# Kernel optimization log

Measured on AMD Instinct MI355X. Metric: run time of the kernel, lower is better.

Reference implementation:

```python
import jax, jax.numpy as jnp
import numpy as np

SPARSITY = 0.8
NEG_INF = -1e10


def setup_inputs() -> dict:
    key = jax.random.key(0)
    k1, k2 = jax.random.split(key)
    B, N, C = 8, 2048, 768
    x = jax.random.normal(k1, (B, N, C), dtype=jnp.float32)
    # torch nn.Linear weight layout: [out_features, in_features] = [3C, C]
    Wqkv = jax.random.normal(k2, (3 * C, C), dtype=jnp.float32) * (1.0 / np.sqrt(C))
    return {"x": x, "Wqkv": Wqkv}


def reference(x, Wqkv):
    B, N, C = x.shape
    qkv = jnp.einsum('bnc,dc->bnd', x, Wqkv)  # [B, N, 3C]
    Q, K, V = jnp.split(qkv, 3, axis=-1)
    attn = jnp.einsum('bnc,bmc->bnm', Q, K) / jnp.sqrt(jnp.float32(C))  # [B,N,N]
    k = int(N * SPARSITY)
    _, idx = jax.lax.top_k(attn, k)  # [B, N, k]
    b_ix = jnp.arange(B)[:, None, None]
    n_ix = jnp.arange(N)[None, :, None]
    mask = jnp.zeros((B, N, N), dtype=bool).at[b_ix, n_ix, idx].set(True)
    attn = jnp.where(mask, attn, jnp.float32(NEG_INF))
    attn = jax.nn.softmax(attn, axis=-1)
    return jnp.einsum('bnm,bmc->bnc', attn, V)
```

## Files before the change

kernel.cpp:

```cpp
#include <hip/hip_runtime.h>
#include <hip/hip_bf16.h>
#include <math.h>


#define BM 256
#define BN 256
#define BK 64
#define NTHREADS 512

typedef __attribute__((ext_vector_type(8))) short bf16x8;
typedef __attribute__((ext_vector_type(4))) float f32x4;

__device__ __forceinline__ unsigned short f2bf(float f) {
    unsigned u = __float_as_uint(f);
    unsigned r = u + 0x7FFFu + ((u >> 16) & 1u);
    return (unsigned short)(r >> 16);
}
__device__ __forceinline__ float bf2f(unsigned short h) {
    return __uint_as_float(((unsigned)h) << 16);
}

__device__ __forceinline__ void async16(const void* g, void* l) {
    __builtin_amdgcn_global_load_lds(
        (const __attribute__((address_space(1))) void*)g,
        (__attribute__((address_space(3))) void*)l, 16, 0, 0);
}

struct GemmArgs {
    const unsigned short* A0;
    const unsigned short* B0;
    const unsigned short* A0b;
    int zsplit;
    int lda, ldb;
    long batchA, batchB;
    int K;
    float alpha;
};

template <int EPI>
__global__ __launch_bounds__(NTHREADS) void gemm_bf16(
    GemmArgs g, void* Cp0, int ldc, long batchC)
{
    __shared__ unsigned short As[2][BM * BK];
    __shared__ unsigned short Bs[2][BM * BK];

    const int t    = threadIdx.x;
    const int wid  = t >> 6, lane = t & 63;
    const int wr   = wid >> 2, wc = wid & 3;
    const int fr   = lane & 15, fq = lane >> 4;
    const int m0   = blockIdx.y * BM, n0 = blockIdx.x * BN;
    const int z    = blockIdx.z;

    const unsigned short* gA0 = g.A0;
    long zA = (long)z * g.batchA;
    if (g.zsplit && z >= g.zsplit) { gA0 = g.A0b; zA = (long)(z - g.zsplit) * g.batchA; }
    const long zB = (long)z * g.batchB;

    const int srow  = wid * 8 + (lane >> 3);
    const int sgcol = ((lane & 7) ^ (lane >> 3)) * 8;

    f32x4 acc[8][4];
#pragma unroll
    for (int m = 0; m < 8; ++m)
#pragma unroll
        for (int n = 0; n < 4; ++n) acc[m][n] = (f32x4)0.f;

    const int nt = g.K / BK;

    int  sg  = 0;
    long sk0 = 0;
    const unsigned short* sA = gA0 + zA + (long)m0 * g.lda;
    const unsigned short* sB = g.B0 + zB + (long)n0 * g.ldb;

    auto STAGE_GROUP = [&]() {
        if (sg < 4 * nt) {
            const int u  = (sg >> 2) & 1;
            const int gp = sg & 3;
            if (gp < 2) {
                char* lb = (char*)&Bs[u][0] + wid * 1024 + gp * 16384;
                const unsigned short* pb = sB + sk0 + sgcol;
                async16(pb + (long)(srow + gp * 128     ) * g.ldb, lb);
                async16(pb + (long)(srow + gp * 128 + 64) * g.ldb, lb + 8192);
            } else {
                const int ap = gp - 2;
                char* la = (char*)&As[u][0] + wid * 1024 + ap * 16384;
                const unsigned short* pa = sA + sk0 + sgcol;
                async16(pa + (long)(srow + ap * 128     ) * g.lda, la);
                async16(pa + (long)(srow + ap * 128 + 64) * g.lda, la + 8192);
            }
            ++sg;
            if ((sg & 3) == 0) sk0 += BK;
        }
    };

    STAGE_GROUP(); STAGE_GROUP(); STAGE_GROUP();
    STAGE_GROUP(); STAGE_GROUP(); STAGE_GROUP();
    asm volatile("s_waitcnt vmcnt(4)" ::: "memory");
    __builtin_amdgcn_sched_barrier(0);
    __builtin_amdgcn_s_barrier();
    __builtin_amdgcn_sched_barrier(0);

    bf16x8 fA[4][2], fB[4][2];

    for (int tt = 0; tt < nt; ++tt) {
        const unsigned short* Ab = &As[tt & 1][0];
        const unsigned short* Bb = &Bs[tt & 1][0];

        auto LDA4 = [&](int mbase) {
#pragma unroll
            for (int mi = 0; mi < 4; ++mi) {
                const int rr = wr * 128 + (mbase + mi) * 16 + fr;
                fA[mi][0] = *(const bf16x8*)&Ab[rr * 64 + ((fq    ) ^ (rr & 7)) * 8];
                fA[mi][1] = *(const bf16x8*)&Ab[rr * 64 + ((fq + 4) ^ (rr & 7)) * 8];
            }
        };
        auto LDB2 = [&](int nbase) {
#pragma unroll
            for (int ni = 0; ni < 2; ++ni) {
                const int rr = wc * 64 + (nbase + ni) * 16 + fr;
                fB[nbase + ni][0] = *(const bf16x8*)&Bb[rr * 64 + ((fq    ) ^ (rr & 7)) * 8];
                fB[nbase + ni][1] = *(const bf16x8*)&Bb[rr * 64 + ((fq + 4) ^ (rr & 7)) * 8];
            }
        };
        auto MFMA16 = [&](int mq, int nq) {
            __builtin_amdgcn_s_setprio(1);
#pragma unroll
            for (int mi = 0; mi < 4; ++mi)
#pragma unroll
                for (int ni = 0; ni < 2; ++ni)
#pragma unroll
                    for (int ks = 0; ks < 2; ++ks)
                        acc[mq * 4 + mi][nq * 2 + ni] =
                            __builtin_amdgcn_mfma_f32_16x16x32_bf16(
                                fA[mi][ks], fB[nq * 2 + ni][ks],
                                acc[mq * 4 + mi][nq * 2 + ni], 0, 0, 0);
            __builtin_amdgcn_s_setprio(0);
        };
        auto BAR = [&]() {
            __builtin_amdgcn_sched_barrier(0);
            __builtin_amdgcn_s_barrier();
            __builtin_amdgcn_sched_barrier(0);
        };
        auto LGKM0 = [&]() {
            asm volatile("s_waitcnt lgkmcnt(0)" ::: "memory");
            __builtin_amdgcn_sched_barrier(0);
        };

        LDA4(0); LDB2(0);
        STAGE_GROUP();
        BAR(); LGKM0();
        MFMA16(0, 0);
        BAR();

        LDB2(2);
        STAGE_GROUP();
        BAR(); LGKM0();
        MFMA16(0, 1);
        BAR();

        LDA4(4);
        STAGE_GROUP();
        BAR(); LGKM0();
        MFMA16(1, 0);
        BAR();

        STAGE_GROUP();
        BAR();
        MFMA16(1, 1);
        if (tt >= nt - 2) {
            asm volatile("s_waitcnt vmcnt(0)" ::: "memory");
        } else {
            asm volatile("s_waitcnt vmcnt(4)" ::: "memory");
        }
        BAR();
    }

#pragma unroll
    for (int m = 0; m < 8; ++m) {
        const int gr0 = m0 + wr * 128 + m * 16 + fq * 4;
#pragma unroll
        for (int n = 0; n < 4; ++n) {
            const int gc = n0 + wc * 64 + n * 16 + fr;
            if (EPI == 0) {
                float* Cf = (float*)Cp0 + (long)z * batchC;
#pragma unroll
                for (int j = 0; j < 4; ++j)
                    Cf[(long)(gr0 + j) * ldc + gc] = g.alpha * acc[m][n][j];
            } else if (EPI == 3) {
                unsigned short* H = (unsigned short*)Cp0;
#pragma unroll
                for (int j = 0; j < 4; ++j)
                    H[(long)(gr0 + j) * ldc + gc] = f2bf(acc[m][n][j]);
            } else if (EPI == 4) {
                unsigned short* H = (unsigned short*)Cp0 + (long)z * batchC;
#pragma unroll
                for (int j = 0; j < 4; ++j)
                    H[(long)(gr0 + j) * ldc + gc] = f2bf(g.alpha * acc[m][n][j]);
            } else {
                unsigned short* Vt = (unsigned short*)Cp0;
                ushort4 p;
                p.x = f2bf(acc[m][n][0]); p.y = f2bf(acc[m][n][1]);
                p.z = f2bf(acc[m][n][2]); p.w = f2bf(acc[m][n][3]);
                const long idx = ((long)(gr0 >> 11) * 768 + gc) * 2048 + (gr0 & 2047);
                *(ushort4*)&Vt[idx] = p;
            }
        }
    }
}

__global__ __launch_bounds__(256) void cast_bf16(
    const float* __restrict__ in, unsigned short* __restrict__ outp, int n8)
{
    const int i = blockIdx.x * 256 + threadIdx.x;
    if (i >= n8) return;
    const float4 a = ((const float4*)in)[i * 2];
    const float4 b = ((const float4*)in)[i * 2 + 1];
    ushort4 h0, h1;
    h0.x = f2bf(a.x); h0.y = f2bf(a.y); h0.z = f2bf(a.z); h0.w = f2bf(a.w);
    h1.x = f2bf(b.x); h1.y = f2bf(b.y); h1.z = f2bf(b.z); h1.w = f2bf(b.w);
    ((ushort4*)outp)[i * 2]     = h0;
    ((ushort4*)outp)[i * 2 + 1] = h1;
}

#define ROWN 2048

__global__ __launch_bounds__(256) void topk_softmax_rows(
    const unsigned short* __restrict__ Sb, unsigned short* __restrict__ P,
    int kkeep)
{
    __shared__ __align__(16) unsigned hist[2048];
    __shared__ float    redmax[4], redmin[4], ssum[4];
    __shared__ unsigned wsum[4];
    __shared__ unsigned selBin;

    const unsigned short* row = Sb + (long)blockIdx.x * ROWN;
    unsigned short* prow = P + (long)blockIdx.x * ROWN;
    const int t    = threadIdx.x;
    const int lane = t & 63, w = t >> 6;

    float x[8];
    {
        const ushort4 a = ((const ushort4*)row)[t * 2];
        const ushort4 b = ((const ushort4*)row)[t * 2 + 1];
        x[0] = bf2f(a.x); x[1] = bf2f(a.y); x[2] = bf2f(a.z); x[3] = bf2f(a.w);
        x[4] = bf2f(b.x); x[5] = bf2f(b.y); x[6] = bf2f(b.z); x[7] = bf2f(b.w);
    }
    ((uint4*)hist)[t * 2]     = make_uint4(0, 0, 0, 0);
    ((uint4*)hist)[t * 2 + 1] = make_uint4(0, 0, 0, 0);

    float mx = x[0], mn = x[0];
#pragma unroll
    for (int j = 1; j < 8; ++j) { mx = fmaxf(mx, x[j]); mn = fminf(mn, x[j]); }
#pragma unroll
    for (int off = 32; off >= 1; off >>= 1) {
        mx = fmaxf(mx, __shfl_xor(mx, off, 64));
        mn = fminf(mn, __shfl_xor(mn, off, 64));
    }
    if (lane == 0) { redmax[w] = mx; redmin[w] = mn; }
    __syncthreads();
    mx = fmaxf(fmaxf(redmax[0], redmax[1]), fmaxf(redmax[2], redmax[3]));
    mn = fminf(fminf(redmin[0], redmin[1]), fminf(redmin[2], redmin[3]));

    const float scale = 2047.0f / fmaxf(mx - mn, 1e-30f);
    int q[8];
#pragma unroll
    for (int j = 0; j < 8; ++j) {
        int v = (int)((x[j] - mn) * scale);
        q[j] = v < 0 ? 0 : (v > 2047 ? 2047 : v);
        atomicAdd(&hist[q[j]], 1u);
    }
    __syncthreads();

    const uint4 h0 = ((const uint4*)hist)[t * 2];
    const uint4 h1 = ((const uint4*)hist)[t * 2 + 1];
    const unsigned hv[8] = { h0.x, h0.y, h0.z, h0.w, h1.x, h1.y, h1.z, h1.w };
    unsigned loc = 0;
#pragma unroll
    for (int j = 0; j < 8; ++j) loc += hv[j];
    unsigned s = loc;
#pragma unroll
    for (int off = 1; off <= 32; off <<= 1) {
        const unsigned o = __shfl_down(s, off, 64);
        s += (lane + off < 64) ? o : 0u;
    }
    if (lane == 0) wsum[w] = s;
    const unsigned texcl = s - loc;
    __syncthreads();
    unsigned above = texcl;
#pragma unroll
    for (int w2 = 0; w2 < 4; ++w2)
        if (w2 > w) above += wsum[w2];
    {
        unsigned cum = above;
        int hit = -1;
#pragma unroll
        for (int j = 7; j >= 0; --j) {
            const unsigned sp = cum;
            cum += hv[j];
            if (cum >= (unsigned)kkeep && sp < (unsigned)kkeep) hit = 8 * t + j;
        }
        if (hit >= 0) selBin = (unsigned)hit;
    }
    __syncthreads();
    const int bstar = (int)selBin;

    float e[8];
    float sum = 0.f;
#pragma unroll
    for (int j = 0; j < 8; ++j) {
        e[j] = (q[j] >= bstar) ? __expf(x[j] - mx) : 0.f;
        sum += e[j];
    }
#pragma unroll
    for (int off = 32; off >= 1; off >>= 1)
        sum += __shfl_xor(sum, off, 64);
    if (lane == 0) ssum[w] = sum;
    __syncthreads();
    const float inv = 1.0f / (ssum[0] + ssum[1] + ssum[2] + ssum[3]);

    ushort4 o0, o1;
    o0.x = f2bf(e[0] * inv); o0.y = f2bf(e[1] * inv);
    o0.z = f2bf(e[2] * inv); o0.w = f2bf(e[3] * inv);
    o1.x = f2bf(e[4] * inv); o1.y = f2bf(e[5] * inv);
    o1.z = f2bf(e[6] * inv); o1.w = f2bf(e[7] * inv);
    ((ushort4*)prow)[t * 2]     = o0;
    ((ushort4*)prow)[t * 2 + 1] = o1;
}

extern "C" void kernel_launch(void* const* d_in, const int* in_sizes, int n_in,
                              void* d_out, int out_size, void* d_ws, size_t ws_size,
                              hipStream_t stream)
{
    const float* x = (const float*)d_in[0];
    const float* W = (const float*)d_in[1];
    float* out = (float*)d_out;

    const int B = 8, N = 2048, C = 768;
    const int M = B * N;
    const int kkeep = 1638;

    char* ws = (char*)d_ws;
    unsigned short* QKb = (unsigned short*)(ws);
    unsigned short* Vt  = (unsigned short*)(ws + 50331648);
    unsigned short* Sb  = (unsigned short*)(ws + 75497472);
    unsigned short* Pb1 = (unsigned short*)(ws + 109051904);
    unsigned short* Pb2 = (unsigned short*)(ws + 142606336);
    unsigned short* xb  = (unsigned short*)(ws + 75497472);
    unsigned short* Wb  = (unsigned short*)(ws + 75497472 + 25165824);

    cast_bf16<<<dim3(M * C / 8 / 256), 256, 0, stream>>>(x, xb, M * C / 8);
    cast_bf16<<<dim3(3 * C * C / 8 / 256), 256, 0, stream>>>(W, Wb, 3 * C * C / 8);

    {
        GemmArgs pa{};
        pa.lda = C; pa.ldb = C; pa.batchA = 0; pa.batchB = 0;
        pa.K = C; pa.alpha = 1.f; pa.zsplit = 0;
        pa.A0 = xb; pa.B0 = Wb;
        gemm_bf16<3><<<dim3(1536 / BN, M / BM, 1), NTHREADS, 0, stream>>>(
            pa, QKb, 1536, 0);
    }
    {
        GemmArgs pv{};
        pv.lda = C; pv.ldb = C; pv.batchA = 0; pv.batchB = 0;
        pv.K = C; pv.alpha = 1.f; pv.zsplit = 0;
        pv.A0 = xb; pv.B0 = Wb + (size_t)1536 * C;
        gemm_bf16<2><<<dim3(C / BN, M / BM, 1), NTHREADS, 0, stream>>>(
            pv, Vt, 0, 0);
    }
    for (int h = 0; h < 2; ++h) {
        const size_t ho = (size_t)h * 4 * N * 1536;
        GemmArgs qk{};
        qk.lda = 1536; qk.ldb = 1536;
        qk.batchA = (long)N * 1536; qk.batchB = (long)N * 1536; qk.K = C;
        qk.alpha = 1.0f / sqrtf((float)C); qk.zsplit = 0;
        qk.A0 = QKb + ho;
        qk.B0 = QKb + ho + C;
        gemm_bf16<4><<<dim3(N / BN, N / BM, 4), NTHREADS, 0, stream>>>(
            qk, Sb, N, (long)N * N);

        topk_softmax_rows<<<dim3(4 * N), 256, 0, stream>>>(
            Sb, h == 0 ? Pb1 : Pb2, kkeep);
    }
    {
        GemmArgs pvv{};
        pvv.lda = N; pvv.ldb = N;
        pvv.batchA = (long)N * N; pvv.batchB = (long)C * N; pvv.K = N;
        pvv.alpha = 1.f;
        pvv.A0 = Pb1; pvv.A0b = Pb2; pvv.zsplit = 4;
        pvv.B0 = Vt;
        gemm_bf16<0><<<dim3(C / BN, N / BM, 8), NTHREADS, 0, stream>>>(
            pvv, out, C, (long)N * C);
    }
}
```

Baseline: 289.2 us.

## Shrink GEMM tiles to 128x128, fuse QKV projection, add XCD block swizzle

Replaces the 256x256, 8-wave GEMM with a simpler 128x128, 4-wave double-buffered kernel and remaps workgroup IDs round-robin across eight groups, likely to spread tiles across XCDs. The Q/K and V projections are merged into one launch, with an epilogue that writes Q/K row-major and V transposed. The two half-batch QK/top-k passes become a single 8-batch launch of each. This cuts launch count and raises block counts for occupancy, but loses the finer-grained interleaved staging and the larger per-block reuse of the old kernel.

```diff
diff --git a/kernel.cpp b/kernel.cpp
--- a/kernel.cpp
+++ b/kernel.cpp
@@ -3,10 +3,9 @@
 #include <math.h>
 
 
-#define BM 256
-#define BN 256
+#define BM 128
+#define BN 128
 #define BK 64
-#define NTHREADS 512
 
 typedef __attribute__((ext_vector_type(8))) short bf16x8;
 typedef __attribute__((ext_vector_type(4))) float f32x4;
@@ -29,8 +28,6 @@
 struct GemmArgs {
     const unsigned short* A0;
     const unsigned short* B0;
-    const unsigned short* A0b;
-    int zsplit;
     int lda, ldb;
     long batchA, batchB;
     int K;
@@ -38,171 +35,129 @@
 };
 
 template <int EPI>
-__global__ __launch_bounds__(NTHREADS) void gemm_bf16(
-    GemmArgs g, void* Cp0, int ldc, long batchC)
+__global__ __launch_bounds__(256) void gemm_bf16(
+    GemmArgs g, void* Cp0, void* Cp1, int ldc, long batchC)
 {
     __shared__ unsigned short As[2][BM * BK];
-    __shared__ unsigned short Bs[2][BM * BK];
+    __shared__ unsigned short Bs[2][BN * BK];
+
+    const int nx  = gridDim.x, ny = gridDim.y;
+    const int nwg = nx * ny * gridDim.z;
+    const int flat = blockIdx.x + nx * (blockIdx.y + ny * blockIdx.z);
+    const int lid  = (flat & 7) * (nwg >> 3) + (flat >> 3);
+    const int bx   = lid % nx;
+    const int byz  = lid / nx;
+    const int by   = byz % ny;
+    const int bz   = byz / ny;
 
     const int t    = threadIdx.x;
     const int wid  = t >> 6, lane = t & 63;
-    const int wr   = wid >> 2, wc = wid & 3;
+    const int wr   = wid >> 1, wc = wid & 1;
     const int fr   = lane & 15, fq = lane >> 4;
-    const int m0   = blockIdx.y * BM, n0 = blockIdx.x * BN;
-    const int z    = blockIdx.z;
-
-    const unsigned short* gA0 = g.A0;
-    long zA = (long)z * g.batchA;
-    if (g.zsplit && z >= g.zsplit) { gA0 = g.A0b; zA = (long)(z - g.zsplit) * g.batchA; }
-    const long zB = (long)z * g.batchB;
-
-    const int srow  = wid * 8 + (lane >> 3);
-    const int sgcol = ((lane & 7) ^ (lane >> 3)) * 8;
-
-    f32x4 acc[8][4];
-#pragma unroll
-    for (int m = 0; m < 8; ++m)
+    const int m0   = by * BM, n0 = bx * BN;
+
+    const unsigned short* Ab0 = g.A0 + (long)bz * g.batchA + (long)m0 * g.lda;
+    const unsigned short* Bb0 = g.B0 + (long)bz * g.batchB + (long)n0 * g.ldb;
+
+    const int srow = t >> 3;
+    const int sgc  = ((t & 7) ^ (srow & 7)) * 8;
+
+    f32x4 acc[4][4];
+#pragma unroll
+    for (int m = 0; m < 4; ++m)
 #pragma unroll
         for (int n = 0; n < 4; ++n) acc[m][n] = (f32x4)0.f;
 
     const int nt = g.K / BK;
 
-    int  sg  = 0;
-    long sk0 = 0;
-    const unsigned short* sA = gA0 + zA + (long)m0 * g.lda;
-    const unsigned short* sB = g.B0 + zB + (long)n0 * g.ldb;
-
-    auto STAGE_GROUP = [&]() {
-        if (sg < 4 * nt) {
-            const int u  = (sg >> 2) & 1;
-            const int gp = sg & 3;
-            if (gp < 2) {
-                char* lb = (char*)&Bs[u][0] + wid * 1024 + gp * 16384;
-                const unsigned short* pb = sB + sk0 + sgcol;
-                async16(pb + (long)(srow + gp * 128     ) * g.ldb, lb);
-                async16(pb + (long)(srow + gp * 128 + 64) * g.ldb, lb + 8192);
-            } else {
-                const int ap = gp - 2;
-                char* la = (char*)&As[u][0] + wid * 1024 + ap * 16384;
-                const unsigned short* pa = sA + sk0 + sgcol;
-                async16(pa + (long)(srow + ap * 128     ) * g.lda, la);
-                async16(pa + (long)(srow + ap * 128 + 64) * g.lda, la + 8192);
-            }
-            ++sg;
-            if ((sg & 3) == 0) sk0 += BK;
+    auto STAGE = [&](int kt, int u) {
+        const long ko = (long)kt * BK + sgc;
+#pragma unroll
+        for (int i = 0; i < 4; ++i) {
+            async16(Ab0 + (long)(i * 32 + srow) * g.lda + ko,
+                    (char*)&As[u][0] + i * 4096 + wid * 1024);
+            async16(Bb0 + (long)(i * 32 + srow) * g.ldb + ko,
+                    (char*)&Bs[u][0] + i * 4096 + wid * 1024);
         }
     };
 
-    STAGE_GROUP(); STAGE_GROUP(); STAGE_GROUP();
-    STAGE_GROUP(); STAGE_GROUP(); STAGE_GROUP();
-    asm volatile("s_waitcnt vmcnt(4)" ::: "memory");
-    __builtin_amdgcn_sched_barrier(0);
-    __builtin_amdgcn_s_barrier();
-    __builtin_amdgcn_sched_barrier(0);
-
-    bf16x8 fA[4][2], fB[4][2];
+    STAGE(0, 0);
 
     for (int tt = 0; tt < nt; ++tt) {
-        const unsigned short* Ab = &As[tt & 1][0];
-        const unsigned short* Bb = &Bs[tt & 1][0];
-
-        auto LDA4 = [&](int mbase) {
-#pragma unroll
-            for (int mi = 0; mi < 4; ++mi) {
-                const int rr = wr * 128 + (mbase + mi) * 16 + fr;
-                fA[mi][0] = *(const bf16x8*)&Ab[rr * 64 + ((fq    ) ^ (rr & 7)) * 8];
-                fA[mi][1] = *(const bf16x8*)&Ab[rr * 64 + ((fq + 4) ^ (rr & 7)) * 8];
-            }
-        };
-        auto LDB2 = [&](int nbase) {
-#pragma unroll
-            for (int ni = 0; ni < 2; ++ni) {
-                const int rr = wc * 64 + (nbase + ni) * 16 + fr;
-                fB[nbase + ni][0] = *(const bf16x8*)&Bb[rr * 64 + ((fq    ) ^ (rr & 7)) * 8];
-                fB[nbase + ni][1] = *(const bf16x8*)&Bb[rr * 64 + ((fq + 4) ^ (rr & 7)) * 8];
-            }
-        };
-        auto MFMA16 = [&](int mq, int nq) {
-            __builtin_amdgcn_s_setprio(1);
-#pragma unroll
-            for (int mi = 0; mi < 4; ++mi)
-#pragma unroll
-                for (int ni = 0; ni < 2; ++ni)
-#pragma unroll
-                    for (int ks = 0; ks < 2; ++ks)
-                        acc[mq * 4 + mi][nq * 2 + ni] =
-                            __builtin_amdgcn_mfma_f32_16x16x32_bf16(
-                                fA[mi][ks], fB[nq * 2 + ni][ks],
-                                acc[mq * 4 + mi][nq * 2 + ni], 0, 0, 0);
-            __builtin_amdgcn_s_setprio(0);
-        };
-        auto BAR = [&]() {
-            __builtin_amdgcn_sched_barrier(0);
-            __builtin_amdgcn_s_barrier();
-            __builtin_amdgcn_sched_barrier(0);
-        };
-        auto LGKM0 = [&]() {
-            asm volatile("s_waitcnt lgkmcnt(0)" ::: "memory");
-            __builtin_amdgcn_sched_barrier(0);
-        };
-
-        LDA4(0); LDB2(0);
-        STAGE_GROUP();
-        BAR(); LGKM0();
-        MFMA16(0, 0);
-        BAR();
-
-        LDB2(2);
-        STAGE_GROUP();
-        BAR(); LGKM0();
-        MFMA16(0, 1);
-        BAR();
-
-        LDA4(4);
-        STAGE_GROUP();
-        BAR(); LGKM0();
-        MFMA16(1, 0);
-        BAR();
-
-        STAGE_GROUP();
-        BAR();
-        MFMA16(1, 1);
-        if (tt >= nt - 2) {
+        const int cur = tt & 1;
+        if (tt + 1 < nt) {
+            STAGE(tt + 1, cur ^ 1);
+            asm volatile("s_waitcnt vmcnt(8)" ::: "memory");
+        } else {
             asm volatile("s_waitcnt vmcnt(0)" ::: "memory");
-        } else {
-            asm volatile("s_waitcnt vmcnt(4)" ::: "memory");
-        }
-        BAR();
-    }
-
-#pragma unroll
-    for (int m = 0; m < 8; ++m) {
-        const int gr0 = m0 + wr * 128 + m * 16 + fq * 4;
+        }
+        __builtin_amdgcn_sched_barrier(0);
+        __builtin_amdgcn_s_barrier();
+        __builtin_amdgcn_sched_barrier(0);
+
+        const unsigned short* Ab = &As[cur][0];
+        const unsigned short* Bb = &Bs[cur][0];
+        bf16x8 fA[4][2], fB[4][2];
+#pragma unroll
+        for (int m = 0; m < 4; ++m) {
+            const int rr = wr * 64 + m * 16 + fr;
+#pragma unroll
+            for (int ks = 0; ks < 2; ++ks)
+                fA[m][ks] = *(const bf16x8*)&Ab[rr * 64 + ((ks * 4 + fq) ^ (rr & 7)) * 8];
+        }
+#pragma unroll
+        for (int n = 0; n < 4; ++n) {
+            const int rr = wc * 64 + n * 16 + fr;
+#pragma unroll
+            for (int ks = 0; ks < 2; ++ks)
+                fB[n][ks] = *(const bf16x8*)&Bb[rr * 64 + ((ks * 4 + fq) ^ (rr & 7)) * 8];
+        }
+        __builtin_amdgcn_s_setprio(1);
+#pragma unroll
+        for (int m = 0; m < 4; ++m)
+#pragma unroll
+            for (int n = 0; n < 4; ++n)
+#pragma unroll
+                for (int ks = 0; ks < 2; ++ks)
+                    acc[m][n] = __builtin_amdgcn_mfma_f32_16x16x32_bf16(
+                        fA[m][ks], fB[n][ks], acc[m][n], 0, 0, 0);
+        __builtin_amdgcn_s_setprio(0);
+        __builtin_amdgcn_sched_barrier(0);
+        __builtin_amdgcn_s_barrier();
+        __builtin_amdgcn_sched_barrier(0);
+    }
+
+#pragma unroll
+    for (int m = 0; m < 4; ++m) {
+        const int gr0 = m0 + wr * 64 + m * 16 + fq * 4;
 #pragma unroll
         for (int n = 0; n < 4; ++n) {
             const int gc = n0 + wc * 64 + n * 16 + fr;
             if (EPI == 0) {
-                float* Cf = (float*)Cp0 + (long)z * batchC;
+                float* Cf = (float*)Cp0 + (long)bz * batchC;
 #pragma unroll
                 for (int j = 0; j < 4; ++j)
                     Cf[(long)(gr0 + j) * ldc + gc] = g.alpha * acc[m][n][j];
-            } else if (EPI == 3) {
-                unsigned short* H = (unsigned short*)Cp0;
-#pragma unroll
-                for (int j = 0; j < 4; ++j)
-                    H[(long)(gr0 + j) * ldc + gc] = f2bf(acc[m][n][j]);
             } else if (EPI == 4) {
-                unsigned short* H = (unsigned short*)Cp0 + (long)z * batchC;
+                unsigned short* H = (unsigned short*)Cp0 + (long)bz * batchC;
 #pragma unroll
                 for (int j = 0; j < 4; ++j)
                     H[(long)(gr0 + j) * ldc + gc] = f2bf(g.alpha * acc[m][n][j]);
             } else {
-                unsigned short* Vt = (unsigned short*)Cp0;
-                ushort4 p;
-                p.x = f2bf(acc[m][n][0]); p.y = f2bf(acc[m][n][1]);
-                p.z = f2bf(acc[m][n][2]); p.w = f2bf(acc[m][n][3]);
-                const long idx = ((long)(gr0 >> 11) * 768 + gc) * 2048 + (gr0 & 2047);
-                *(ushort4*)&Vt[idx] = p;
+                if (n0 < 1536) {
+                    unsigned short* H = (unsigned short*)Cp0;
+#pragma unroll
+                    for (int j = 0; j < 4; ++j)
+                        H[(long)(gr0 + j) * ldc + gc] = f2bf(acc[m][n][j]);
+                } else {
+                    unsigned short* Vt = (unsigned short*)Cp1;
+                    ushort4 p;
+                    p.x = f2bf(acc[m][n][0]); p.y = f2bf(acc[m][n][1]);
+                    p.z = f2bf(acc[m][n][2]); p.w = f2bf(acc[m][n][3]);
+                    const long idx =
+                        ((long)(gr0 >> 11) * 768 + (gc - 1536)) * 2048 + (gr0 & 2047);
+                    *(ushort4*)&Vt[idx] = p;
+                }
             }
         }
     }
@@ -343,52 +298,39 @@
     unsigned short* QKb = (unsigned short*)(ws);
     unsigned short* Vt  = (unsigned short*)(ws + 50331648);
     unsigned short* Sb  = (unsigned short*)(ws + 75497472);
-    unsigned short* Pb1 = (unsigned short*)(ws + 109051904);
-    unsigned short* Pb2 = (unsigned short*)(ws + 142606336);
+    unsigned short* Pb  = (unsigned short*)(ws + 142606336);
     unsigned short* xb  = (unsigned short*)(ws + 75497472);
-    unsigned short* Wb  = (unsigned short*)(ws + 75497472 + 25165824);
+    unsigned short* Wb  = (unsigned short*)(ws + 100663296);
 
     cast_bf16<<<dim3(M * C / 8 / 256), 256, 0, stream>>>(x, xb, M * C / 8);
     cast_bf16<<<dim3(3 * C * C / 8 / 256), 256, 0, stream>>>(W, Wb, 3 * C * C / 8);
 
     {
         GemmArgs pa{};
+        pa.A0 = xb; pa.B0 = Wb;
         pa.lda = C; pa.ldb = C; pa.batchA = 0; pa.batchB = 0;
-        pa.K = C; pa.alpha = 1.f; pa.zsplit = 0;
-        pa.A0 = xb; pa.B0 = Wb;
-        gemm_bf16<3><<<dim3(1536 / BN, M / BM, 1), NTHREADS, 0, stream>>>(
-            pa, QKb, 1536, 0);
-    }
+        pa.K = C; pa.alpha = 1.f;
+        gemm_bf16<5><<<dim3(2304 / BN, M / BM, 1), 256, 0, stream>>>(
+            pa, QKb, Vt, 1536, 0);
+    }
+    {
+        GemmArgs qk{};
+        qk.A0 = QKb; qk.B0 = QKb + C;
+        qk.lda = 1536; qk.ldb = 1536;
+        qk.batchA = (long)N * 1536; qk.batchB = (long)N * 1536;
+        qk.K = C; qk.alpha = 1.0f / sqrtf((float)C);
+        gemm_bf16<4><<<dim3(N / BN, N / BM, 8), 256, 0, stream>>>(
+            qk, Sb, nullptr, N, (long)N * N);
+    }
+    topk_softmax_rows<<<dim3(B * N), 256, 0, stream>>>(Sb, Pb, kkeep);
+
     {
         GemmArgs pv{};
-        pv.lda = C; pv.ldb = C; pv.batchA = 0; pv.batchB = 0;
-        pv.K = C; pv.alpha = 1.f; pv.zsplit = 0;
-        pv.A0 = xb; pv.B0 = Wb + (size_t)1536 * C;
-        gemm_bf16<2><<<dim3(C / BN, M / BM, 1), NTHREADS, 0, stream>>>(
-            pv, Vt, 0, 0);
-    }
-    for (int h = 0; h < 2; ++h) {
-        const size_t ho = (size_t)h * 4 * N * 1536;
-        GemmArgs qk{};
-        qk.lda = 1536; qk.ldb = 1536;
-        qk.batchA = (long)N * 1536; qk.batchB = (long)N * 1536; qk.K = C;
-        qk.alpha = 1.0f / sqrtf((float)C); qk.zsplit = 0;
-        qk.A0 = QKb + ho;
-        qk.B0 = QKb + ho + C;
-        gemm_bf16<4><<<dim3(N / BN, N / BM, 4), NTHREADS, 0, stream>>>(
-            qk, Sb, N, (long)N * N);
-
-        topk_softmax_rows<<<dim3(4 * N), 256, 0, stream>>>(
-            Sb, h == 0 ? Pb1 : Pb2, kkeep);
-    }
-    {
-        GemmArgs pvv{};
-        pvv.lda = N; pvv.ldb = N;
-        pvv.batchA = (long)N * N; pvv.batchB = (long)C * N; pvv.K = N;
-        pvv.alpha = 1.f;
-        pvv.A0 = Pb1; pvv.A0b = Pb2; pvv.zsplit = 4;
-        pvv.B0 = Vt;
-        gemm_bf16<0><<<dim3(C / BN, N / BM, 8), NTHREADS, 0, stream>>>(
-            pvv, out, C, (long)N * C);
-    }
-}
+        pv.A0 = Pb; pv.B0 = Vt;
+        pv.lda = N; pv.ldb = N;
+        pv.batchA = (long)N * N; pv.batchB = (long)C * N;
+        pv.K = N; pv.alpha = 1.f;
+        gemm_bf16<0><<<dim3(C / BN, N / BM, 8), 256, 0, stream>>>(
+            pv, out, nullptr, C, (long)N * C);
+    }
+}
```

Measured after the change: 267.8 us. 1.08x faster.
